# Performance work log

Measured on AMD Instinct MI355X. Metric: run time of the kernel, lower is better.

The kernel has to match this reference:

```python
import jax, jax.numpy as jnp
import numpy as np

B, N, P, D = 16, 358, 72, 96
ND, H, K = 64, 4, 10
HL = H // 2
HG = H - HL
NH = 4  # temporal attention heads


def ln(x, g, b, eps=1e-5):
    m = x.mean(-1, keepdims=True)
    v = ((x - m) ** 2).mean(-1, keepdims=True)
    return (x - m) / jnp.sqrt(v + eps) * g + b


def topk_sparsify(adj, k):
    # row-wise top-k masking + renormalization, vectorized over all leading dims
    shp = adj.shape
    n = shp[-1]
    flat = adj.reshape(-1, shp[-2], n)
    M, R = flat.shape[0], flat.shape[1]
    _, idx = jax.lax.top_k(flat, k)  # (M,R,k)
    mask = jnp.zeros(flat.shape, flat.dtype).at[
        jnp.arange(M)[:, None, None], jnp.arange(R)[None, :, None], idx].set(1.0)
    sp = flat * mask
    sp = sp / (sp.sum(-1, keepdims=True) + 1e-8)
    return sp.reshape(shp)


def forward(patch_features, local_e1, local_e2, global_e1, global_e2, static_e2,
            temperature, pos_enc, wq, bq, wk, bk, wv, bv, wo, bo, tn_g, tn_b,
            de_w1, de_b1, de_g1, de_beta1, de_w2, de_b2, de_g2, de_beta2,
            gnn_w, gnn_b, gnn_g, gnn_beta, gf_w, gf_b,
            ee_w1, ee_b1, ee_g, ee_beta, ee_w2, ee_b2, ee_w3, ee_b3):
    # ---- static multi-head graphs (batched over heads instead of python loop) ----
    adj_l = jax.nn.relu(jnp.einsum('hnd,hdm->hnm', local_e1, local_e2))
    t_l = jnp.clip(temperature[:HL] * 2.0, 0.1, 5.0)
    adj_l = jax.nn.softmax(adj_l / t_l[:, None, None], axis=-1)
    adj_g = jax.nn.relu(jnp.einsum('hnd,hdm->hnm', global_e1, global_e2))
    t_g = jnp.clip(temperature[HL:] * 0.5, 0.1, 2.0)
    adj_g = jax.nn.softmax(adj_g / t_g[:, None, None], axis=-1)
    static_adjs = jnp.concatenate([adj_l, adj_g], axis=0)  # (H,N,N)

    # ---- dynamic graphs ----
    b, n, p, d = patch_features.shape
    pr = patch_features.reshape(b * n, p, d)
    x = pr + pos_enc[:, :p]
    hd = d // NH
    q = (x @ wq + bq).reshape(-1, p, NH, hd).transpose(0, 2, 1, 3)
    kk = (x @ wk + bk).reshape(-1, p, NH, hd).transpose(0, 2, 1, 3)
    v = (x @ wv + bv).reshape(-1, p, NH, hd).transpose(0, 2, 1, 3)
    att = jax.nn.softmax(jnp.einsum('bhqd,bhkd->bhqk', q, kk) / np.float32(np.sqrt(hd)), axis=-1)
    o = jnp.einsum('bhqk,bhkd->bhqd', att, v).transpose(0, 2, 1, 3).reshape(-1, p, d)
    attended = o @ wo + bo  # (BN,P,D)
    imp = jax.nn.softmax(attended.mean(-1), axis=1)  # (BN,P)
    node = (attended * imp[..., None]).sum(1) + pr.mean(1)
    node = ln(node, tn_g, tn_b).reshape(b, n, d)
    h1 = jax.nn.gelu(ln(node @ de_w1 + de_b1, de_g1, de_beta1), approximate=False)
    dyn = ln(h1 @ de_w2 + de_b2, de_g2, de_beta2)  # (B,N,ND)
    for i in range(2):  # 2 structurally distinct GNN layers, batched over B
        sim = jax.nn.softmax(jnp.einsum('bnd,bmd->bnm', dyn, dyn) / 0.2, axis=-1)
        agg = jnp.einsum('bnm,bmd->bnd', sim, dyn)
        out = jax.nn.gelu(ln(agg @ gnn_w[i] + gnn_b[i], gnn_g[i], gnn_beta[i]), approximate=False)
        dyn = out + dyn
    dsim = jax.nn.relu(jnp.einsum('bnd,hdm->bhnm', dyn, static_e2))
    t_d = jnp.clip(temperature, 0.1, 2.0)
    dynamic_adjs = jax.nn.softmax(dsim / t_d[None, :, None, None], axis=-1)  # (B,H,N,N)

    static_adjs = topk_sparsify(static_adjs, K)
    dynamic_adjs = topk_sparsify(dynamic_adjs, K)

    # ---- static/dynamic fusion ----
    node_f = patch_features.mean(2)  # (B,N,D)
    fw = jax.nn.sigmoid(node_f @ gf_w + gf_b)  # (B,N,H)
    w = jnp.transpose(fw, (0, 2, 1))[..., None]  # (B,H,N,1), broadcast over columns
    fused = (1.0 - w) * static_adjs[None] + w * dynamic_adjs  # (B,H,N,N)

    # ---- edge encoder over head dim ----
    mh = jnp.transpose(fused, (0, 2, 3, 1))  # (B,N,N,H)
    e = jax.nn.gelu(ln(mh @ ee_w1 + ee_b1, ee_g, ee_beta), approximate=False)
    e = jax.nn.gelu(e @ ee_w2 + ee_b2, approximate=False)
    e = (e @ ee_w3 + ee_b3)[..., 0]  # (B,N,N)
    final = jax.nn.sigmoid(e) * fused.mean(1)
    return final, static_adjs, dynamic_adjs


def setup_inputs() -> dict:
    key = jax.random.key(0)
    ks = jax.random.split(key, 20)
    r = lambda i, shape, s=0.05: jax.random.normal(ks[i], shape, dtype=jnp.float32) * s
    z = lambda shape: jnp.zeros(shape, jnp.float32)
    o = lambda shape: jnp.ones(shape, jnp.float32)
    return dict(
        patch_features=r(0, (B, N, P, D), 1.0),
        local_e1=r(1, (HL, N, ND // 2), 0.1),
        local_e2=r(2, (HL, ND // 2, N), 0.1),
        global_e1=r(3, (HG, N, ND), 0.1),
        global_e2=r(4, (HG, ND, N), 0.1),
        static_e2=r(5, (H, ND, N), 0.1),
        temperature=jnp.full((H,), 0.5, jnp.float32),
        pos_enc=r(6, (1, 72, D), 0.02),
        wq=r(7, (D, D)), bq=z((D,)),
        wk=r(8, (D, D)), bk=z((D,)),
        wv=r(9, (D, D)), bv=z((D,)),
        wo=r(10, (D, D)), bo=z((D,)),
        tn_g=o((D,)), tn_b=z((D,)),
        de_w1=r(11, (D, 2 * ND)), de_b1=z((2 * ND,)),
        de_g1=o((2 * ND,)), de_beta1=z((2 * ND,)),
        de_w2=r(12, (2 * ND, ND)), de_b2=z((ND,)),
        de_g2=o((ND,)), de_beta2=z((ND,)),
        gnn_w=r(13, (2, ND, ND)), gnn_b=z((2, ND)),
        gnn_g=o((2, ND)), gnn_beta=z((2, ND)),
        gf_w=r(14, (D, H)), gf_b=z((H,)),
        ee_w1=r(15, (H, 4 * H)), ee_b1=z((4 * H,)),
        ee_g=o((4 * H,)), ee_beta=z((4 * H,)),
        ee_w2=r(16, (4 * H, 2 * H)), ee_b2=z((2 * H,)),
        ee_w3=r(17, (2 * H, 1)), ee_b3=z((1,)),
    )


def reference(patch_features, local_e1, local_e2, global_e1, global_e2, static_e2,
              temperature, pos_enc, wq, bq, wk, bk, wv, bv, wo, bo, tn_g, tn_b,
              de_w1, de_b1, de_g1, de_beta1, de_w2, de_b2, de_g2, de_beta2,
              gnn_w, gnn_b, gnn_g, gnn_beta, gf_w, gf_b,
              ee_w1, ee_b1, ee_g, ee_beta, ee_w2, ee_b2, ee_w3, ee_b3):
    return forward(patch_features, local_e1, local_e2, global_e1, global_e2, static_e2,
                   temperature, pos_enc, wq, bq, wk, bk, wv, bv, wo, bo, tn_g, tn_b,
                   de_w1, de_b1, de_g1, de_beta1, de_w2, de_b2, de_g2, de_beta2,
                   gnn_w, gnn_b, gnn_g, gnn_beta, gf_w, gf_b,
                   ee_w1, ee_b1, ee_g, ee_beta, ee_w2, ee_b2, ee_w3, ee_b3)
```

## Files before the change

kernel.cpp:

```cpp
#include <hip/hip_runtime.h>
#include <hip/hip_bf16.h>

#define B_ 16
#define N_ 358
#define P_ 72
#define D_ 96
#define ND_ 64
#define H_ 4
#define NH_ 4
#define HD_ 24
#define K_ 10
#define BN_ (B_*N_)
#define NN_ (N_*N_)
#define RPW_ 6

__device__ __forceinline__ float gelu_f(float x){ return 0.5f*x*(1.0f+erff(x*0.7071067811865476f)); }
__device__ __forceinline__ float sigm_f(float x){ return 1.0f/(1.0f+expf(-x)); }

__global__ __launch_bounds__(256) void attn_kernel(
    const float* __restrict__ patch, const float* __restrict__ pos,
    const float* __restrict__ wq, const float* __restrict__ bq,
    const float* __restrict__ wk, const float* __restrict__ bk,
    const float* __restrict__ wv, const float* __restrict__ bv,
    const float* __restrict__ wo, const float* __restrict__ bo,
    const float* __restrict__ tng, const float* __restrict__ tnb,
    float* __restrict__ node_out, float* __restrict__ meanpr_out)
{
    __shared__ float smem[10656];
    __shared__ float rr[P_];
    __shared__ float nb[D_];
    __shared__ float st2[2];

    float* const xs  = smem;
    float* const qh  = smem;
    float* const kh  = smem + 1800;
    float* const vh  = smem + 3600;
    float* const att = smem + 5400;
    float* const ats = smem;

    const int tid = threadIdx.x;
    const int tc  = tid & 31;
    const int tr  = tid >> 5;
    const int rbase = tr * 9;
    const int bn  = blockIdx.x;
    const float* pr = patch + (size_t)bn * (P_*D_);

    float mpr = 0.f;
    if (tid < D_) {
        for (int p = 0; p < P_; ++p) mpr += pr[p*D_+tid];
        mpr *= (1.0f/P_);
        meanpr_out[(size_t)bn*D_ + tid] = mpr;
    }

    for (int e = tid; e < P_*D_; e += 256) {
        int row = e / D_, col = e - row*D_;
        xs[row*97 + col] = pr[e] + pos[e];
    }
    __syncthreads();

    float aq[3][9], ak[3][9], av[3][9];
    #pragma unroll
    for (int j = 0; j < 3; ++j) {
        const int c = tc + 32*j;
        const float vbq = bq[c], vbk = bk[c], vbv = bv[c];
        #pragma unroll
        for (int i = 0; i < 9; ++i) { aq[j][i]=vbq; ak[j][i]=vbk; av[j][i]=vbv; }
    }
    for (int k = 0; k < D_; ++k) {
        float xv[9];
        #pragma unroll
        for (int i = 0; i < 9; ++i) xv[i] = xs[(rbase+i)*97 + k];
        const float* wqp = wq + k*D_;
        const float* wkp = wk + k*D_;
        const float* wvp = wv + k*D_;
        float wqv[3], wkv[3], wvv[3];
        #pragma unroll
        for (int j = 0; j < 3; ++j) {
            const int c = tc + 32*j;
            wqv[j]=wqp[c]; wkv[j]=wkp[c]; wvv[j]=wvp[c];
        }
        #pragma unroll
        for (int j = 0; j < 3; ++j)
            #pragma unroll
            for (int i = 0; i < 9; ++i) {
                aq[j][i] += xv[i]*wqv[j];
                ak[j][i] += xv[i]*wkv[j];
                av[j][i] += xv[i]*wvv[j];
            }
    }
    __syncthreads();

    float ao[3][9];
    #pragma unroll
    for (int j = 0; j < 3; ++j) {
        const float vbo = bo[tc + 32*j];
        #pragma unroll
        for (int i = 0; i < 9; ++i) ao[j][i] = vbo;
    }

    const float rs = 0.20412414523193154f;
    for (int h = 0; h < NH_; ++h) {
        #pragma unroll
        for (int j = 0; j < 3; ++j) {
            const int c = tc + 32*j;
            const int dl = c - HD_*h;
            if ((unsigned)dl < (unsigned)HD_) {
                #pragma unroll
                for (int i = 0; i < 9; ++i) {
                    qh[(rbase+i)*25 + dl] = aq[j][i];
                    kh[(rbase+i)*25 + dl] = ak[j][i];
                    vh[(rbase+i)*25 + dl] = av[j][i];
                }
            }
        }
        __syncthreads();

        {
            float sc[3][9];
            #pragma unroll
            for (int jj = 0; jj < 3; ++jj)
                #pragma unroll
                for (int i = 0; i < 9; ++i) sc[jj][i] = 0.f;
            for (int d = 0; d < HD_; ++d) {
                float qv[9];
                #pragma unroll
                for (int i = 0; i < 9; ++i) qv[i] = qh[(rbase+i)*25 + d];
                float kv[3];
                #pragma unroll
                for (int jj = 0; jj < 3; ++jj) {
                    const int jn = tc + 32*jj;
                    kv[jj] = (jn < P_) ? kh[jn*25 + d] : 0.f;
                }
                #pragma unroll
                for (int jj = 0; jj < 3; ++jj)
                    #pragma unroll
                    for (int i = 0; i < 9; ++i) sc[jj][i] += qv[i]*kv[jj];
            }
            #pragma unroll
            for (int jj = 0; jj < 3; ++jj) {
                const int jn = tc + 32*jj;
                if (jn < P_) {
                    #pragma unroll
                    for (int i = 0; i < 9; ++i)
                        att[(rbase+i)*73 + jn] = sc[jj][i]*rs;
                }
            }
        }
        __syncthreads();

        if (tid < P_) {
            float* ar = att + tid*73;
            float mx = ar[0];
            for (int j = 1; j < P_; ++j) mx = fmaxf(mx, ar[j]);
            float sm = 0.f;
            for (int j = 0; j < P_; ++j) { float ev = expf(ar[j]-mx); ar[j]=ev; sm += ev; }
            float inv = 1.0f/sm;
            for (int j = 0; j < P_; ++j) ar[j] *= inv;
        }
        __syncthreads();

        if (tc < HD_) {
            float ov[9];
            #pragma unroll
            for (int i = 0; i < 9; ++i) ov[i] = 0.f;
            for (int j = 0; j < P_; ++j) {
                const float vv = vh[j*25 + tc];
                #pragma unroll
                for (int i = 0; i < 9; ++i) ov[i] += att[(rbase+i)*73 + j]*vv;
            }
            #pragma unroll
            for (int i = 0; i < 9; ++i) kh[(rbase+i)*25 + tc] = ov[i];
        }
        __syncthreads();

        for (int d = 0; d < HD_; ++d) {
            float ovv[9];
            #pragma unroll
            for (int i = 0; i < 9; ++i) ovv[i] = kh[(rbase+i)*25 + d];
            const float* wop = wo + (HD_*h + d)*D_;
            float wv3[3];
            #pragma unroll
            for (int j = 0; j < 3; ++j) wv3[j] = wop[tc + 32*j];
            #pragma unroll
            for (int j = 0; j < 3; ++j)
                #pragma unroll
                for (int i = 0; i < 9; ++i) ao[j][i] += ovv[i]*wv3[j];
        }
        __syncthreads();
    }

    #pragma unroll
    for (int j = 0; j < 3; ++j) {
        const int c = tc + 32*j;
        #pragma unroll
        for (int i = 0; i < 9; ++i) ats[(rbase+i)*97 + c] = ao[j][i];
    }
    __syncthreads();

    if (tid < P_) {
        const float* ar = ats + tid*97;
        float s = 0.f;
        for (int d = 0; d < D_; ++d) s += ar[d];
        rr[tid] = s*(1.0f/D_);
    }
    __syncthreads();
    if (tid == 0) {
        float mx = rr[0];
        for (int i=1;i<P_;++i) mx = fmaxf(mx, rr[i]);
        float sm=0.f;
        for (int i=0;i<P_;++i){ float ev=expf(rr[i]-mx); rr[i]=ev; sm+=ev; }
        float inv=1.0f/sm;
        for (int i=0;i<P_;++i) rr[i]*=inv;
    }
    __syncthreads();
    if (tid < D_) {
        float s = 0.f;
        for (int i=0;i<P_;++i) s += ats[i*97+tid]*rr[i];
        nb[tid] = s + mpr;
    }
    __syncthreads();
    if (tid == 0) {
        float m=0.f; for(int d=0;d<D_;++d) m+=nb[d]; m *= (1.0f/D_);
        float v=0.f; for(int d=0;d<D_;++d){ float df=nb[d]-m; v+=df*df; } v *= (1.0f/D_);
        st2[0]=m; st2[1]=rsqrtf(v+1e-5f);
    }
    __syncthreads();
    if (tid < D_) {
        float y = (nb[tid]-st2[0])*st2[1]*tng[tid] + tnb[tid];
        node_out[(size_t)bn*D_+tid] = y;
    }
}

__global__ __launch_bounds__(128) void enc1_kernel(
    const float* __restrict__ node, const float* __restrict__ w1, const float* __restrict__ b1,
    const float* __restrict__ g1, const float* __restrict__ be1, float* __restrict__ h1)
{
    __shared__ float nr[D_];
    __shared__ float buf[128];
    __shared__ float st2[2];
    const int tid = threadIdx.x; const int bn = blockIdx.x;
    if (tid < D_) nr[tid] = node[(size_t)bn*D_+tid];
    __syncthreads();
    float s = b1[tid];
    for (int c = 0; c < D_; ++c) s += nr[c]*w1[c*128+tid];
    buf[tid] = s;
    __syncthreads();
    if (tid == 0) {
        float m=0.f; for(int d=0;d<128;++d) m+=buf[d]; m *= (1.0f/128.0f);
        float v=0.f; for(int d=0;d<128;++d){ float df=buf[d]-m; v+=df*df; } v *= (1.0f/128.0f);
        st2[0]=m; st2[1]=rsqrtf(v+1e-5f);
    }
    __syncthreads();
    float y = (buf[tid]-st2[0])*st2[1]*g1[tid] + be1[tid];
    h1[(size_t)bn*128+tid] = gelu_f(y);
}

__global__ __launch_bounds__(64) void enc2_kernel(
    const float* __restrict__ h1, const float* __restrict__ w2, const float* __restrict__ b2,
    const float* __restrict__ g2, const float* __restrict__ be2, float* __restrict__ dyn)
{
    __shared__ float hr[128];
    __shared__ float buf[ND_];
    __shared__ float st2[2];
    const int tid = threadIdx.x; const int bn = blockIdx.x;
    hr[tid] = h1[(size_t)bn*128+tid];
    hr[tid+64] = h1[(size_t)bn*128+64+tid];
    __syncthreads();
    float s = b2[tid];
    for (int c = 0; c < 128; ++c) s += hr[c]*w2[c*ND_+tid];
    buf[tid] = s;
    __syncthreads();
    if (tid == 0) {
        float m=0.f; for(int d=0;d<ND_;++d) m+=buf[d]; m *= (1.0f/ND_);
        float v=0.f; for(int d=0;d<ND_;++d){ float df=buf[d]-m; v+=df*df; } v *= (1.0f/ND_);
        st2[0]=m; st2[1]=rsqrtf(v+1e-5f);
    }
    __syncthreads();
    dyn[(size_t)bn*ND_+tid] = (buf[tid]-st2[0])*st2[1]*g2[tid] + be2[tid];
}

__global__ __launch_bounds__(256) void gnn_kernel(
    const float* __restrict__ din, float* __restrict__ dout,
    const float* __restrict__ gw, const float* __restrict__ gb,
    const float* __restrict__ gg, const float* __restrict__ gbe, int layer)
{
    __shared__ float dq[ND_];
    __shared__ float prob[N_];
    __shared__ float red[256];
    __shared__ float aggp[4*ND_];
    __shared__ float buf[ND_];
    __shared__ float st2[2];
    const int tid = threadIdx.x; const int bn = blockIdx.x;
    const int b = bn / N_;
    const float* base = din + (size_t)b*N_*ND_;
    if (tid < ND_) dq[tid] = din[(size_t)bn*ND_+tid];
    __syncthreads();

    float lmax = -1e30f;
    for (int m = tid; m < N_; m += 256) {
        const float* rm = base + (size_t)m*ND_;
        float s = 0.f;
        for (int c = 0; c < ND_; ++c) s += dq[c]*rm[c];
        s *= 5.0f;
        prob[m] = s;
        lmax = fmaxf(lmax, s);
    }
    red[tid]=lmax; __syncthreads();
    for (int st=128; st>0; st>>=1){ if(tid<st) red[tid]=fmaxf(red[tid],red[tid+st]); __syncthreads(); }
    const float mx = red[0]; __syncthreads();
    float lsum = 0.f;
    for (int m=tid; m<N_; m+=256){ float ev=expf(prob[m]-mx); prob[m]=ev; lsum+=ev; }
    red[tid]=lsum; __syncthreads();
    for (int st=128; st>0; st>>=1){ if(tid<st) red[tid]+=red[tid+st]; __syncthreads(); }
    const float inv = 1.0f/red[0]; __syncthreads();
    for (int m=tid; m<N_; m+=256) prob[m]*=inv;
    __syncthreads();

    {
        const int part = tid >> 6, d = tid & 63;
        float s = 0.f;
        for (int m = part; m < N_; m += 4) s += prob[m]*base[(size_t)m*ND_+d];
        aggp[part*ND_+d] = s;
    }
    __syncthreads();
    if (tid < ND_)
        aggp[tid] = aggp[tid]+aggp[ND_+tid]+aggp[2*ND_+tid]+aggp[3*ND_+tid];
    __syncthreads();
    if (tid < ND_) {
        float t = gb[layer*ND_+tid];
        for (int c = 0; c < ND_; ++c) t += aggp[c]*gw[(layer*ND_+c)*ND_+tid];
        buf[tid] = t;
    }
    __syncthreads();
    if (tid == 0) {
        float m=0.f; for(int d=0;d<ND_;++d) m+=buf[d]; m *= (1.0f/ND_);
        float v=0.f; for(int d=0;d<ND_;++d){ float df=buf[d]-m; v+=df*df; } v *= (1.0f/ND_);
        st2[0]=m; st2[1]=rsqrtf(v+1e-5f);
    }
    __syncthreads();
    if (tid < ND_) {
        float y = (buf[tid]-st2[0])*st2[1]*gg[layer*ND_+tid] + gbe[layer*ND_+tid];
        dout[(size_t)bn*ND_+tid] = gelu_f(y) + dq[tid];
    }
}

__device__ __forceinline__ void wave_softmax_topk_store(
    float lv[RPW_], int lane, float* __restrict__ outrow)
{
    float mx = 0.f;
    #pragma unroll
    for (int j=0;j<RPW_;++j) mx = fmaxf(mx, lv[j]);
    #pragma unroll
    for (int s=1;s<64;s<<=1) mx = fmaxf(mx, __shfl_xor(mx, s));
    float sm = 0.f;
    #pragma unroll
    for (int j=0;j<RPW_;++j) {
        const int m = lane + 64*j;
        const float e = (m < N_) ? expf(lv[j]-mx) : 0.f;
        lv[j] = e; sm += e;
    }
    #pragma unroll
    for (int s=1;s<64;s<<=1) sm += __shfl_xor(sm, s);
    const float inv = 1.0f/sm;
    #pragma unroll
    for (int j=0;j<RPW_;++j) lv[j] *= inv;

    unsigned sel = 0u;
    float ksum = 0.f;
    for (int it = 0; it < K_; ++it) {
        float bv = -1.f; int bm = 0x7fffffff;
        #pragma unroll
        for (int j=0;j<RPW_;++j) {
            const int m = lane + 64*j;
            if (m < N_ && !((sel>>j)&1u) && lv[j] > bv) { bv = lv[j]; bm = m; }
        }
        #pragma unroll
        for (int s=1;s<64;s<<=1) {
            const float ov = __shfl_xor(bv, s);
            const int   om = __shfl_xor(bm, s);
            if (ov > bv || (ov == bv && om < bm)) { bv = ov; bm = om; }
        }
        ksum += bv;
        if ((bm & 63) == lane) sel |= 1u << (bm >> 6);
    }
    const float dn = 1.0f/(ksum + 1e-8f);
    #pragma unroll
    for (int j=0;j<RPW_;++j) {
        const int m = lane + 64*j;
        if (m < N_) outrow[m] = ((sel>>j)&1u) ? lv[j]*dn : 0.f;
    }
}

__global__ __launch_bounds__(256) void static_adj_kernel(
    const float* __restrict__ le1, const float* __restrict__ le2,
    const float* __restrict__ ge1, const float* __restrict__ ge2,
    const float* __restrict__ temp, float* __restrict__ outs)
{
    __shared__ float e1l[4][ND_];
    const int tid = threadIdx.x;
    const int wv = tid >> 6, lane = tid & 63;
    const int r = blockIdx.x*4 + wv;
    const int h = r / N_, n = r % N_;
    if (h < 2) { if (lane < 32) e1l[wv][lane] = le1[(h*N_+n)*32+lane]; }
    else       { e1l[wv][lane] = ge1[((h-2)*N_+n)*64+lane]; }
    __syncthreads();
    const float t = temp[h];
    const float tl = (h < 2) ? fminf(fmaxf(t*2.0f,0.1f),5.0f) : fminf(fmaxf(t*0.5f,0.1f),2.0f);
    const float invt = 1.0f/tl;
    float lv[RPW_];
    #pragma unroll
    for (int j=0;j<RPW_;++j) lv[j] = 0.f;
    if (h < 2) {
        for (int c = 0; c < 32; ++c) {
            const float dc = e1l[wv][c];
            const float* sr = le2 + (size_t)(h*32+c)*N_;
            #pragma unroll
            for (int j=0;j<RPW_;++j) {
                const int m = lane + 64*j;
                if (m < N_) lv[j] += dc*sr[m];
            }
        }
    } else {
        for (int c = 0; c < 64; ++c) {
            const float dc = e1l[wv][c];
            const float* sr = ge2 + (size_t)((h-2)*64+c)*N_;
            #pragma unroll
            for (int j=0;j<RPW_;++j) {
                const int m = lane + 64*j;
                if (m < N_) lv[j] += dc*sr[m];
            }
        }
    }
    #pragma unroll
    for (int j=0;j<RPW_;++j) lv[j] = fmaxf(lv[j],0.f)*invt;
    wave_softmax_topk_store(lv, lane, outs + (size_t)r*N_);
}

__global__ __launch_bounds__(256) void dyn_adj_kernel(
    const float* __restrict__ dyn, const float* __restrict__ se2,
    const float* __restrict__ temp, float* __restrict__ outd)
{
    __shared__ float dql[4][ND_];
    const int tid = threadIdx.x;
    const int wv = tid >> 6, lane = tid & 63;
    const int r = blockIdx.x*4 + wv;
    const int b = r / (H_*N_);
    const int rem = r % (H_*N_);
    const int h = rem / N_, n = rem % N_;
    dql[wv][lane] = dyn[((size_t)(b*N_+n))*ND_ + lane];
    __syncthreads();
    const float invt = 1.0f/fminf(fmaxf(temp[h],0.1f),2.0f);
    float lv[RPW_];
    #pragma unroll
    for (int j=0;j<RPW_;++j) lv[j] = 0.f;
    const float* sb = se2 + (size_t)h*ND_*N_;
    for (int c = 0; c < ND_; ++c) {
        const float dc = dql[wv][c];
        const float* sr = sb + (size_t)c*N_;
        #pragma unroll
        for (int j=0;j<RPW_;++j) {
            const int m = lane + 64*j;
            if (m < N_) lv[j] += dc*sr[m];
        }
    }
    #pragma unroll
    for (int j=0;j<RPW_;++j) lv[j] = fmaxf(lv[j],0.f)*invt;
    wave_softmax_topk_store(lv, lane, outd + ((size_t)(b*H_+h)*N_+n)*(size_t)N_);
}

__global__ __launch_bounds__(256) void fw_kernel(
    const float* __restrict__ meanpr, const float* __restrict__ gfw,
    const float* __restrict__ gfb, float* __restrict__ wf)
{
    const int gid = blockIdx.x*256 + threadIdx.x;
    if (gid >= BN_*H_) return;
    const int bn = gid >> 2, h = gid & 3;
    float s = gfb[h];
    const float* mp = meanpr + (size_t)bn*D_;
    for (int c=0;c<D_;++c) s += mp[c]*gfw[c*H_+h];
    wf[gid] = sigm_f(s);
}

__global__ __launch_bounds__(256) void edge_kernel(
    const float* __restrict__ staticf, const float* __restrict__ dynf,
    const float* __restrict__ wf,
    const float* __restrict__ ew1, const float* __restrict__ eb1,
    const float* __restrict__ eg,  const float* __restrict__ ebe,
    const float* __restrict__ ew2, const float* __restrict__ eb2,
    const float* __restrict__ ew3, const float* __restrict__ eb3,
    float* __restrict__ outf)
{
    __shared__ float w1s[64], w2s[128], b1s[16], gs[16], bes[16], b2s[8], w3s[8];
    __shared__ float b3v;
    const int tid = threadIdx.x;
    if (tid < 64)                 w1s[tid]     = ew1[tid];
    else if (tid < 192)           w2s[tid-64]  = ew2[tid-64];
    else if (tid < 208)           b1s[tid-192] = eb1[tid-192];
    else if (tid < 224)           gs[tid-208]  = eg[tid-208];
    else if (tid < 240)           bes[tid-224] = ebe[tid-224];
    else if (tid < 248)           b2s[tid-240] = eb2[tid-240];
    else                          w3s[tid-248] = ew3[tid-248];
    if (tid == 0) b3v = eb3[0];
    __syncthreads();

    const size_t gid = (size_t)blockIdx.x*256 + tid;
    if (gid >= (size_t)B_*NN_) return;
    const int m = (int)(gid % N_);
    const size_t t1 = gid / N_;
    const int n = (int)(t1 % N_);
    const int b = (int)(t1 / N_);

    const float* wrow = wf + ((size_t)(b*N_+n))*4;
    float mh[4]; float msum = 0.f;
    #pragma unroll
    for (int h=0; h<4; ++h) {
        float w  = wrow[h];
        float st = staticf[((size_t)(h*N_+n))*N_ + m];
        float da = dynf[(((size_t)(b*4+h))*N_+n)*(size_t)N_ + m];
        float f = (1.0f-w)*st + w*da;
        mh[h] = f; msum += f;
    }
    float e16[16]; float mean = 0.f;
    #pragma unroll
    for (int j=0;j<16;++j) {
        float s = b1s[j];
        #pragma unroll
        for (int h=0;h<4;++h) s += mh[h]*w1s[h*16+j];
        e16[j] = s; mean += s;
    }
    mean *= (1.0f/16.0f);
    float var = 0.f;
    #pragma unroll
    for (int j=0;j<16;++j){ float df=e16[j]-mean; var += df*df; }
    var *= (1.0f/16.0f);
    const float rinv = rsqrtf(var + 1e-5f);
    #pragma unroll
    for (int j=0;j<16;++j) e16[j] = gelu_f((e16[j]-mean)*rinv*gs[j] + bes[j]);
    float e8[8];
    #pragma unroll
    for (int o=0;o<8;++o) {
        float s = b2s[o];
        #pragma unroll
        for (int j=0;j<16;++j) s += e16[j]*w2s[j*8+o];
        e8[o] = gelu_f(s);
    }
    float e = b3v;
    #pragma unroll
    for (int o=0;o<8;++o) e += e8[o]*w3s[o];
    outf[gid] = sigm_f(e) * (msum*0.25f);
}

extern "C" void kernel_launch(void* const* d_in, const int* in_sizes, int n_in,
                              void* d_out, int out_size, void* d_ws, size_t ws_size,
                              hipStream_t stream)
{
    const float* patch = (const float*)d_in[0];
    const float* le1   = (const float*)d_in[1];
    const float* le2   = (const float*)d_in[2];
    const float* ge1   = (const float*)d_in[3];
    const float* ge2   = (const float*)d_in[4];
    const float* se2   = (const float*)d_in[5];
    const float* temp  = (const float*)d_in[6];
    const float* pos   = (const float*)d_in[7];
    const float* wq    = (const float*)d_in[8];
    const float* bq    = (const float*)d_in[9];
    const float* wk    = (const float*)d_in[10];
    const float* bk    = (const float*)d_in[11];
    const float* wv    = (const float*)d_in[12];
    const float* bv    = (const float*)d_in[13];
    const float* wo    = (const float*)d_in[14];
    const float* bo    = (const float*)d_in[15];
    const float* tng   = (const float*)d_in[16];
    const float* tnb   = (const float*)d_in[17];
    const float* dw1   = (const float*)d_in[18];
    const float* db1   = (const float*)d_in[19];
    const float* dg1   = (const float*)d_in[20];
    const float* dbe1  = (const float*)d_in[21];
    const float* dw2   = (const float*)d_in[22];
    const float* db2   = (const float*)d_in[23];
    const float* dg2   = (const float*)d_in[24];
    const float* dbe2  = (const float*)d_in[25];
    const float* gw    = (const float*)d_in[26];
    const float* gb    = (const float*)d_in[27];
    const float* gg    = (const float*)d_in[28];
    const float* gbe   = (const float*)d_in[29];
    const float* gfw   = (const float*)d_in[30];
    const float* gfb   = (const float*)d_in[31];
    const float* ew1   = (const float*)d_in[32];
    const float* eb1   = (const float*)d_in[33];
    const float* eg    = (const float*)d_in[34];
    const float* ebe   = (const float*)d_in[35];
    const float* ew2   = (const float*)d_in[36];
    const float* eb2   = (const float*)d_in[37];
    const float* ew3   = (const float*)d_in[38];
    const float* eb3   = (const float*)d_in[39];
    (void)in_sizes; (void)n_in; (void)out_size; (void)ws_size;

    float* ws      = (float*)d_ws;
    float* meanpr  = ws;
    float* node    = meanpr + (size_t)BN_*D_;
    float* h1      = node   + (size_t)BN_*D_;
    float* dyn0    = h1     + (size_t)BN_*128;
    float* dyn1    = node;
    float* wfuse   = h1;

    float* out        = (float*)d_out;
    float* out_final  = out;
    float* out_static = out + (size_t)B_*NN_;
    float* out_dyn    = out_static + (size_t)H_*NN_;

    attn_kernel<<<BN_, 256, 0, stream>>>(patch,pos,wq,bq,wk,bk,wv,bv,wo,bo,tng,tnb,node,meanpr);
    enc1_kernel<<<BN_, 128, 0, stream>>>(node,dw1,db1,dg1,dbe1,h1);
    enc2_kernel<<<BN_, 64,  0, stream>>>(h1,dw2,db2,dg2,dbe2,dyn0);
    gnn_kernel<<<BN_, 256, 0, stream>>>(dyn0,dyn1,gw,gb,gg,gbe,0);
    gnn_kernel<<<BN_, 256, 0, stream>>>(dyn1,dyn0,gw,gb,gg,gbe,1);
    static_adj_kernel<<<H_*N_/4, 256, 0, stream>>>(le1,le2,ge1,ge2,temp,out_static);
    dyn_adj_kernel<<<B_*H_*N_/4, 256, 0, stream>>>(dyn0,se2,temp,out_dyn);
    fw_kernel<<<(BN_*H_+255)/256, 256, 0, stream>>>(meanpr,gfw,gfb,wfuse);
    edge_kernel<<<((size_t)B_*NN_+255)/256, 256, 0, stream>>>(
        out_static,out_dyn,wfuse,ew1,eb1,eg,ebe,ew2,eb2,ew3,eb3,out_final);
}
```

Baseline: 2.869 ms.

## Restructure temporal attention kernel: 512 threads, vectorized LDS, warp-level softmax

```diff
diff --git a/kernel.cpp b/kernel.cpp
--- a/kernel.cpp
+++ b/kernel.cpp
@@ -13,11 +13,12 @@
 #define BN_ (B_*N_)
 #define NN_ (N_*N_)
 #define RPW_ 6
+#define NR5 5
 
 __device__ __forceinline__ float gelu_f(float x){ return 0.5f*x*(1.0f+erff(x*0.7071067811865476f)); }
 __device__ __forceinline__ float sigm_f(float x){ return 1.0f/(1.0f+expf(-x)); }
 
-__global__ __launch_bounds__(256) void attn_kernel(
+__global__ __launch_bounds__(512, 4) void attn_kernel(
     const float* __restrict__ patch, const float* __restrict__ pos,
     const float* __restrict__ wq, const float* __restrict__ bq,
     const float* __restrict__ wk, const float* __restrict__ bk,
@@ -26,22 +27,23 @@
     const float* __restrict__ tng, const float* __restrict__ tnb,
     float* __restrict__ node_out, float* __restrict__ meanpr_out)
 {
-    __shared__ float smem[10656];
-    __shared__ float rr[P_];
+    __shared__ __align__(16) float pool[14808];
+    __shared__ float rr[80];
     __shared__ float nb[D_];
     __shared__ float st2[2];
 
-    float* const xs  = smem;
-    float* const qh  = smem;
-    float* const kh  = smem + 1800;
-    float* const vh  = smem + 3600;
-    float* const att = smem + 5400;
-    float* const ats = smem;
+    float* const xs   = pool;
+    float* const qh   = pool;
+    float* const khT  = pool + 2240;
+    float* const vhT  = pool + 4568;
+    float* const att  = pool + 6488;
+    float* const obuf = pool + 12568;
+    float* const ats  = pool;
 
     const int tid = threadIdx.x;
     const int tc  = tid & 31;
     const int tr  = tid >> 5;
-    const int rbase = tr * 9;
+    const int rbase = tr * NR5;
     const int bn  = blockIdx.x;
     const float* pr = patch + (size_t)bn * (P_*D_);
 
@@ -52,140 +54,165 @@
         meanpr_out[(size_t)bn*D_ + tid] = mpr;
     }
 
-    for (int e = tid; e < P_*D_; e += 256) {
-        int row = e / D_, col = e - row*D_;
-        xs[row*97 + col] = pr[e] + pos[e];
-    }
-    __syncthreads();
-
-    float aq[3][9], ak[3][9], av[3][9];
+    for (int e = tid; e < 80*100; e += 512) {
+        const int row = e / 100, col = e - row*100;
+        xs[e] = (row < P_ && col < D_) ? (pr[row*D_+col] + pos[row*D_+col]) : 0.f;
+    }
+    __syncthreads();
+
+    float aq[3][NR5], ak[3][NR5], av[3][NR5];
     #pragma unroll
     for (int j = 0; j < 3; ++j) {
         const int c = tc + 32*j;
         const float vbq = bq[c], vbk = bk[c], vbv = bv[c];
         #pragma unroll
-        for (int i = 0; i < 9; ++i) { aq[j][i]=vbq; ak[j][i]=vbk; av[j][i]=vbv; }
-    }
-    for (int k = 0; k < D_; ++k) {
-        float xv[9];
-        #pragma unroll
-        for (int i = 0; i < 9; ++i) xv[i] = xs[(rbase+i)*97 + k];
-        const float* wqp = wq + k*D_;
-        const float* wkp = wk + k*D_;
-        const float* wvp = wv + k*D_;
-        float wqv[3], wkv[3], wvv[3];
+        for (int i = 0; i < NR5; ++i) { aq[j][i]=vbq; ak[j][i]=vbk; av[j][i]=vbv; }
+    }
+
+#define P1_MAT(WP, ACC)                                                      \
+        {                                                                    \
+            float w4[3][4];                                                  \
+            _Pragma("unroll")                                                \
+            for (int j = 0; j < 3; ++j) {                                    \
+                const int c = tc + 32*j;                                     \
+                _Pragma("unroll")                                            \
+                for (int kk = 0; kk < 4; ++kk)                               \
+                    w4[j][kk] = WP[(k0+kk)*D_ + c];                          \
+            }                                                                \
+            _Pragma("unroll")                                                \
+            for (int j = 0; j < 3; ++j)                                      \
+                _Pragma("unroll")                                            \
+                for (int i = 0; i < NR5; ++i)                                \
+                    ACC[j][i] += xv[i].x*w4[j][0] + xv[i].y*w4[j][1]         \
+                               + xv[i].z*w4[j][2] + xv[i].w*w4[j][3];        \
+        }
+
+    for (int k0 = 0; k0 < D_; k0 += 4) {
+        float4 xv[NR5];
+        #pragma unroll
+        for (int i = 0; i < NR5; ++i)
+            xv[i] = *reinterpret_cast<const float4*>(&xs[(rbase+i)*100 + k0]);
+        P1_MAT(wq, aq)
+        P1_MAT(wk, ak)
+        P1_MAT(wv, av)
+    }
+    __syncthreads();
+
+    const float rs = 0.20412414523193154f;
+
+    float ao[3][NR5];
+    #pragma unroll
+    for (int j = 0; j < 3; ++j) {
+        const float vbo = bo[tc + 32*j];
+        #pragma unroll
+        for (int i = 0; i < NR5; ++i) ao[j][i] = vbo;
+    }
+
+    auto stage = [&](int hh) {
         #pragma unroll
         for (int j = 0; j < 3; ++j) {
             const int c = tc + 32*j;
-            wqv[j]=wqp[c]; wkv[j]=wkp[c]; wvv[j]=wvp[c];
-        }
-        #pragma unroll
-        for (int j = 0; j < 3; ++j)
-            #pragma unroll
-            for (int i = 0; i < 9; ++i) {
-                aq[j][i] += xv[i]*wqv[j];
-                ak[j][i] += xv[i]*wkv[j];
-                av[j][i] += xv[i]*wvv[j];
-            }
-    }
-    __syncthreads();
-
-    float ao[3][9];
-    #pragma unroll
-    for (int j = 0; j < 3; ++j) {
-        const float vbo = bo[tc + 32*j];
-        #pragma unroll
-        for (int i = 0; i < 9; ++i) ao[j][i] = vbo;
-    }
-
-    const float rs = 0.20412414523193154f;
-    for (int h = 0; h < NH_; ++h) {
-        #pragma unroll
-        for (int j = 0; j < 3; ++j) {
-            const int c = tc + 32*j;
-            const int dl = c - HD_*h;
+            const int dl = c - HD_*hh;
             if ((unsigned)dl < (unsigned)HD_) {
                 #pragma unroll
-                for (int i = 0; i < 9; ++i) {
-                    qh[(rbase+i)*25 + dl] = aq[j][i];
-                    kh[(rbase+i)*25 + dl] = ak[j][i];
-                    vh[(rbase+i)*25 + dl] = av[j][i];
+                for (int i = 0; i < NR5; ++i) {
+                    const int row = rbase + i;
+                    qh [row*28 + dl] = aq[j][i] * rs;
+                    khT[dl*97 + row] = ak[j][i];
+                    vhT[dl*80 + row] = av[j][i];
                 }
             }
         }
+    };
+
+    stage(0);
+    __syncthreads();
+
+    for (int h = 0; h < NH_; ++h) {
+        float sc[3][NR5];
+        #pragma unroll
+        for (int j = 0; j < 3; ++j)
+            #pragma unroll
+            for (int i = 0; i < NR5; ++i) sc[j][i] = 0.f;
+        for (int d0 = 0; d0 < HD_; d0 += 4) {
+            float4 qv[NR5];
+            #pragma unroll
+            for (int i = 0; i < NR5; ++i)
+                qv[i] = *reinterpret_cast<const float4*>(&qh[(rbase+i)*28 + d0]);
+            float kv[3][4];
+            #pragma unroll
+            for (int j = 0; j < 3; ++j) {
+                const int jn = tc + 32*j;
+                #pragma unroll
+                for (int kk = 0; kk < 4; ++kk)
+                    kv[j][kk] = khT[(d0+kk)*97 + jn];
+            }
+            #pragma unroll
+            for (int j = 0; j < 3; ++j)
+                #pragma unroll
+                for (int i = 0; i < NR5; ++i)
+                    sc[j][i] += qv[i].x*kv[j][0] + qv[i].y*kv[j][1]
+                              + qv[i].z*kv[j][2] + qv[i].w*kv[j][3];
+        }
+
+        #pragma unroll
+        for (int i = 0; i < NR5; ++i) {
+            float m = fmaxf(sc[0][i], sc[1][i]);
+            if (tc < 8) m = fmaxf(m, sc[2][i]);
+            #pragma unroll
+            for (int s = 1; s < 32; s <<= 1) m = fmaxf(m, __shfl_xor(m, s, 32));
+            const float e0 = expf(sc[0][i]-m);
+            const float e1 = expf(sc[1][i]-m);
+            const float e2 = (tc < 8) ? expf(sc[2][i]-m) : 0.f;
+            float sm = e0 + e1 + e2;
+            #pragma unroll
+            for (int s = 1; s < 32; s <<= 1) sm += __shfl_xor(sm, s, 32);
+            const float inv = 1.0f/sm;
+            const int row = rbase + i;
+            att[row*76 + tc]      = e0*inv;
+            att[row*76 + tc + 32] = e1*inv;
+            if (tc < 8) att[row*76 + tc + 64] = e2*inv;
+        }
         __syncthreads();
 
-        {
-            float sc[3][9];
-            #pragma unroll
-            for (int jj = 0; jj < 3; ++jj)
+        if (tc < HD_) {
+            float ov[NR5];
+            #pragma unroll
+            for (int i = 0; i < NR5; ++i) ov[i] = 0.f;
+            for (int j0 = 0; j0 < P_; j0 += 4) {
+                const float4 vv = *reinterpret_cast<const float4*>(&vhT[tc*80 + j0]);
                 #pragma unroll
-                for (int i = 0; i < 9; ++i) sc[jj][i] = 0.f;
-            for (int d = 0; d < HD_; ++d) {
-                float qv[9];
-                #pragma unroll
-                for (int i = 0; i < 9; ++i) qv[i] = qh[(rbase+i)*25 + d];
-                float kv[3];
-                #pragma unroll
-                for (int jj = 0; jj < 3; ++jj) {
-                    const int jn = tc + 32*jj;
-                    kv[jj] = (jn < P_) ? kh[jn*25 + d] : 0.f;
-                }
-                #pragma unroll
-                for (int jj = 0; jj < 3; ++jj)
-                    #pragma unroll
-                    for (int i = 0; i < 9; ++i) sc[jj][i] += qv[i]*kv[jj];
-            }
-            #pragma unroll
-            for (int jj = 0; jj < 3; ++jj) {
-                const int jn = tc + 32*jj;
-                if (jn < P_) {
-                    #pragma unroll
-                    for (int i = 0; i < 9; ++i)
-                        att[(rbase+i)*73 + jn] = sc[jj][i]*rs;
+                for (int i = 0; i < NR5; ++i) {
+                    const float4 pa = *reinterpret_cast<const float4*>(&att[(rbase+i)*76 + j0]);
+                    ov[i] += pa.x*vv.x + pa.y*vv.y + pa.z*vv.z + pa.w*vv.w;
                 }
             }
+            #pragma unroll
+            for (int i = 0; i < NR5; ++i) obuf[(rbase+i)*28 + tc] = ov[i];
         }
         __syncthreads();
 
-        if (tid < P_) {
-            float* ar = att + tid*73;
-            float mx = ar[0];
-            for (int j = 1; j < P_; ++j) mx = fmaxf(mx, ar[j]);
-            float sm = 0.f;
-            for (int j = 0; j < P_; ++j) { float ev = expf(ar[j]-mx); ar[j]=ev; sm += ev; }
-            float inv = 1.0f/sm;
-            for (int j = 0; j < P_; ++j) ar[j] *= inv;
-        }
-        __syncthreads();
-
-        if (tc < HD_) {
-            float ov[9];
-            #pragma unroll
-            for (int i = 0; i < 9; ++i) ov[i] = 0.f;
-            for (int j = 0; j < P_; ++j) {
-                const float vv = vh[j*25 + tc];
+        for (int d0 = 0; d0 < HD_; d0 += 4) {
+            float4 ov4[NR5];
+            #pragma unroll
+            for (int i = 0; i < NR5; ++i)
+                ov4[i] = *reinterpret_cast<const float4*>(&obuf[(rbase+i)*28 + d0]);
+            float w4[3][4];
+            #pragma unroll
+            for (int j = 0; j < 3; ++j) {
+                const int c = tc + 32*j;
                 #pragma unroll
-                for (int i = 0; i < 9; ++i) ov[i] += att[(rbase+i)*73 + j]*vv;
+                for (int kk = 0; kk < 4; ++kk)
+                    w4[j][kk] = wo[(HD_*h + d0 + kk)*D_ + c];
             }
-            #pragma unroll
-            for (int i = 0; i < 9; ++i) kh[(rbase+i)*25 + tc] = ov[i];
-        }
-        __syncthreads();
-
-        for (int d = 0; d < HD_; ++d) {
-            float ovv[9];
-            #pragma unroll
-            for (int i = 0; i < 9; ++i) ovv[i] = kh[(rbase+i)*25 + d];
-            const float* wop = wo + (HD_*h + d)*D_;
-            float wv3[3];
-            #pragma unroll
-            for (int j = 0; j < 3; ++j) wv3[j] = wop[tc + 32*j];
             #pragma unroll
             for (int j = 0; j < 3; ++j)
                 #pragma unroll
-                for (int i = 0; i < 9; ++i) ao[j][i] += ovv[i]*wv3[j];
-        }
+                for (int i = 0; i < NR5; ++i)
+                    ao[j][i] += ov4[i].x*w4[j][0] + ov4[i].y*w4[j][1]
+                              + ov4[i].z*w4[j][2] + ov4[i].w*w4[j][3];
+        }
+        if (h < NH_-1) stage(h+1);
         __syncthreads();
     }
 
@@ -193,40 +220,55 @@
     for (int j = 0; j < 3; ++j) {
         const int c = tc + 32*j;
         #pragma unroll
-        for (int i = 0; i < 9; ++i) ats[(rbase+i)*97 + c] = ao[j][i];
+        for (int i = 0; i < NR5; ++i) ats[(rbase+i)*100 + c] = ao[j][i];
     }
     __syncthreads();
 
     if (tid < P_) {
-        const float* ar = ats + tid*97;
+        const float* ar = ats + tid*100;
         float s = 0.f;
         for (int d = 0; d < D_; ++d) s += ar[d];
         rr[tid] = s*(1.0f/D_);
     }
     __syncthreads();
-    if (tid == 0) {
-        float mx = rr[0];
-        for (int i=1;i<P_;++i) mx = fmaxf(mx, rr[i]);
-        float sm=0.f;
-        for (int i=0;i<P_;++i){ float ev=expf(rr[i]-mx); rr[i]=ev; sm+=ev; }
-        float inv=1.0f/sm;
-        for (int i=0;i<P_;++i) rr[i]*=inv;
+    if (tid < 64) {
+        const float a0 = rr[tid];
+        const float a1 = (tid < 8) ? rr[64+tid] : -3.0e38f;
+        float mx = fmaxf(a0, a1);
+        #pragma unroll
+        for (int s = 1; s < 64; s <<= 1) mx = fmaxf(mx, __shfl_xor(mx, s));
+        const float e0 = expf(a0-mx);
+        const float e1 = (tid < 8) ? expf(a1-mx) : 0.f;
+        float sm = e0 + e1;
+        #pragma unroll
+        for (int s = 1; s < 64; s <<= 1) sm += __shfl_xor(sm, s);
+        const float inv = 1.0f/sm;
+        rr[tid] = e0*inv;
+        if (tid < 8) rr[64+tid] = e1*inv;
     }
     __syncthreads();
     if (tid < D_) {
         float s = 0.f;
-        for (int i=0;i<P_;++i) s += ats[i*97+tid]*rr[i];
+        for (int i = 0; i < P_; ++i) s += ats[i*100+tid]*rr[i];
         nb[tid] = s + mpr;
     }
     __syncthreads();
-    if (tid == 0) {
-        float m=0.f; for(int d=0;d<D_;++d) m+=nb[d]; m *= (1.0f/D_);
-        float v=0.f; for(int d=0;d<D_;++d){ float df=nb[d]-m; v+=df*df; } v *= (1.0f/D_);
-        st2[0]=m; st2[1]=rsqrtf(v+1e-5f);
+    if (tid < 64) {
+        const float x0 = nb[tid];
+        const float x1 = (tid < 32) ? nb[64+tid] : 0.f;
+        float sm = x0 + x1;
+        float sq = x0*x0 + x1*x1;
+        #pragma unroll
+        for (int s = 1; s < 64; s <<= 1) { sm += __shfl_xor(sm, s); sq += __shfl_xor(sq, s); }
+        if (tid == 0) {
+            const float m = sm*(1.0f/D_);
+            const float v = sq*(1.0f/D_) - m*m;
+            st2[0] = m; st2[1] = rsqrtf(v + 1e-5f);
+        }
     }
     __syncthreads();
     if (tid < D_) {
-        float y = (nb[tid]-st2[0])*st2[1]*tng[tid] + tnb[tid];
+        const float y = (nb[tid]-st2[0])*st2[1]*tng[tid] + tnb[tid];
         node_out[(size_t)bn*D_+tid] = y;
     }
 }
@@ -609,7 +651,7 @@
     float* out_static = out + (size_t)B_*NN_;
     float* out_dyn    = out_static + (size_t)H_*NN_;
 
-    attn_kernel<<<BN_, 256, 0, stream>>>(patch,pos,wq,bq,wk,bk,wv,bv,wo,bo,tng,tnb,node,meanpr);
+    attn_kernel<<<BN_, 512, 0, stream>>>(patch,pos,wq,bq,wk,bk,wv,bv,wo,bo,tng,tnb,node,meanpr);
     enc1_kernel<<<BN_, 128, 0, stream>>>(node,dw1,db1,dg1,dbe1,h1);
     enc2_kernel<<<BN_, 64,  0, stream>>>(h1,dw2,db2,dg2,dbe2,dyn0);
     gnn_kernel<<<BN_, 256, 0, stream>>>(dyn0,dyn1,gw,gb,gg,gbe,0);
```

After: 10.61 ms. 3.7x slower.
